# Kernel optimization log

Hardware: AMD Instinct MI355X
Metric: run time of the kernel (lower is better)

Reference implementation:

```python
import jax, jax.numpy as jnp
import numpy as np

B, N, E, H = 8, 2048, 64, 4
D = E * H  # internal width = embedding_dim * num_heads


def _ln(x, g, b):
    m = jnp.mean(x, -1, keepdims=True)
    v = jnp.var(x, -1, keepdims=True)
    return (x - m) / jnp.sqrt(v + 1e-5) * g + b


def setup_inputs() -> dict:
    key = jax.random.key(0)
    ks = jax.random.split(key, 10)

    def lin(k, o, i):
        return jax.random.normal(k, (o, i), jnp.float32) / np.sqrt(i).astype(np.float32)

    return {
        "x": jax.random.normal(ks[0], (B, N, E), jnp.float32),
        "weights": jax.random.uniform(ks[1], (B, N, 1), jnp.float32),
        "ln_g": jnp.ones((E,), jnp.float32),
        "ln_b": jnp.zeros((E,), jnp.float32),
        "wq_w": lin(ks[2], D, E), "wq_b": jnp.zeros((D,), jnp.float32),
        "wk_w": lin(ks[3], D, E), "wk_b": jnp.zeros((D,), jnp.float32),
        "wv_w": lin(ks[4], D, E), "wv_b": jnp.zeros((D,), jnp.float32),
        "mq_w": lin(ks[5], D, D), "mq_b": jnp.zeros((D,), jnp.float32),
        "mk_w": lin(ks[6], D, D), "mk_b": jnp.zeros((D,), jnp.float32),
        "out_w": lin(ks[7], E, D), "out_b": jnp.zeros((E,), jnp.float32),
        "ffn_w": lin(ks[8], E, E), "ffn_b": jnp.zeros((E,), jnp.float32),
    }


def reference(x, weights, ln_g, ln_b, wq_w, wq_b, wk_w, wk_b, wv_w, wv_b,
              mq_w, mq_b, mk_w, mk_b, out_w, out_b, ffn_w, ffn_b):
    Bn, Nn, En = x.shape
    Dd = mq_w.shape[0]
    Hh = Dd // En  # head_dim == embedding_dim in this module

    x_norm = _ln(x, ln_g, ln_b)
    # outer W_q/W_k then nn.MultiheadAttention in-projections (q,k only; v/out_proj are dead)
    q = (x_norm @ wq_w.T + wq_b) @ mq_w.T + mq_b  # [B,N,D]
    k = (x_norm @ wk_w.T + wk_b) @ mk_w.T + mk_b  # [B,N,D]
    q = q.reshape(Bn, Nn, Hh, En)
    k = k.reshape(Bn, Nn, Hh, En)

    scale = np.float32(1.0 / np.sqrt(En))
    scores = jnp.einsum('bihe,bjhe->bhij', q, k) * scale  # [B,H,N,N]
    pad = jnp.sum(weights, -1) == 0.0  # [B,N] key_padding_mask
    scores = jnp.where(pad[:, None, None, :], jnp.float32(-1e9), scores)
    att = jax.nn.softmax(scores, axis=-1).mean(axis=1)  # averaged over heads: [B,N,N]

    # re-weight by input weights and renormalize (second softmax-like pass)
    att = att * weights[..., 0][:, None, :]
    att = att / jnp.sum(att, -1, keepdims=True)

    v = x_norm @ wv_w.T + wv_b  # fresh W_v(x_norm), NOT MHA's value path
    att_out = jnp.einsum('bij,bjd->bid', att, v)  # [B,N,D]

    out1 = x + att_out @ out_w.T + out_b  # [B,N,E]
    out2 = jax.nn.softplus(_ln(out1, ln_g, ln_b) @ ffn_w.T + ffn_b)
    return _ln(out1 + out2, ln_g, ln_b)
```

## Files before the change

kernel.cpp:

```cpp
#include <hip/hip_runtime.h>
#include <hip/hip_bf16.h>

#define BB 8
#define NN 2048
#define EE 64
#define DD 256

typedef __attribute__((ext_vector_type(8))) short short8;
typedef __attribute__((ext_vector_type(4))) float f32x4;
typedef __attribute__((ext_vector_type(4))) unsigned short ushort4v;

#define MFMA16(a, b, c) __builtin_amdgcn_mfma_f32_16x16x32_bf16((a), (b), (c), 0, 0, 0)

#if __has_builtin(__builtin_amdgcn_exp2f)
#define EXP2(x) __builtin_amdgcn_exp2f(x)
#else
#define EXP2(x) exp2f(x)
#endif

__device__ inline void gload16(const void* g, void* l) {
  __builtin_amdgcn_global_load_lds(
      (const __attribute__((address_space(1))) unsigned int*)g,
      (__attribute__((address_space(3))) unsigned int*)l, 16, 0, 0);
}

__device__ inline float bf2f(unsigned short u) {
  union { unsigned int i; float f; } v;
  v.i = ((unsigned int)u) << 16;
  return v.f;
}
__device__ inline unsigned short f2bf(float f) {
  union { float f; unsigned int i; } v;
  v.f = f;
  unsigned int r = v.i + 0x7FFFu + ((v.i >> 16) & 1u);
  return (unsigned short)(r >> 16);
}

__global__ __launch_bounds__(128) void kprep(
    const float* __restrict__ wq_w, const float* __restrict__ wq_b,
    const float* __restrict__ wk_w, const float* __restrict__ wk_b,
    const float* __restrict__ wv_w, const float* __restrict__ mq_w,
    const float* __restrict__ mq_b, const float* __restrict__ mk_w,
    const float* __restrict__ mk_b, const float* __restrict__ out_w,
    const float* __restrict__ ffn_w,
    unsigned short* __restrict__ wqc, float* __restrict__ bqc,
    unsigned short* __restrict__ wkc, float* __restrict__ bkc,
    unsigned short* __restrict__ wvc, unsigned short* __restrict__ outwb,
    unsigned short* __restrict__ ffnwb) {
  const float SC = 0.18033688011112042f;
  int o = blockIdx.x;
  int t = threadIdx.x;
  if (t < 64) {
    float acc = 0.f;
#pragma unroll 4
    for (int d = 0; d < 256; d++) acc += mq_w[o * 256 + d] * wq_w[d * 64 + t];
    wqc[o * 64 + t] = f2bf(acc * SC);
  } else {
    int k = t - 64;
    float acc = 0.f;
#pragma unroll 4
    for (int d = 0; d < 256; d++) acc += mk_w[o * 256 + d] * wk_w[d * 64 + k];
    wkc[o * 64 + k] = f2bf(acc);
  }
  if (t == 0) {
    float acc = 0.f;
    for (int d = 0; d < 256; d++) acc += mq_w[o * 256 + d] * wq_b[d];
    bqc[o] = (acc + mq_b[o]) * SC;
  }
  if (t == 64) {
    float acc = 0.f;
    for (int d = 0; d < 256; d++) acc += mk_w[o * 256 + d] * wk_b[d];
    bkc[o] = acc + mk_b[o];
  }
  int gid = o * 128 + t;
  if (gid < 16384) {
    wvc[gid] = f2bf(wv_w[gid]);
    outwb[gid] = f2bf(out_w[gid]);
  }
  if (gid < 4096) ffnwb[gid] = f2bf(ffn_w[gid]);
}

__global__ __launch_bounds__(128, 2) void kproj(
    const float* __restrict__ x, const float* __restrict__ ln_g,
    const float* __restrict__ ln_b, const unsigned short* __restrict__ wqc,
    const float* __restrict__ bqc, const unsigned short* __restrict__ wkc,
    const float* __restrict__ bkc, const unsigned short* __restrict__ wvc,
    const float* __restrict__ wv_b, unsigned short* __restrict__ qout,
    unsigned short* __restrict__ kout, unsigned short* __restrict__ vtout) {
  __shared__ __align__(1024) char lds[2 * 10240];
  int tid = threadIdx.x;
  int w = tid >> 6, l = tid & 63;
  int c = l & 15, g = l >> 4;
  int blk = blockIdx.x;
  int b = blk >> 6;
  int i0 = (blk & 63) * 32 + w * 16;
  size_t row0 = (size_t)b * NN + i0;
  char* xnb = lds + w * 10240;
  char* tlb = lds + w * 10240 + 2048;

  int rl = l >> 2;
  int cc = (l & 3) * 16;
  float xv[16];
  {
    const float* xr = x + (row0 + rl) * EE + cc;
#pragma unroll
    for (int i = 0; i < 4; i++) {
      float4 v = *(const float4*)(xr + i * 4);
      xv[i * 4 + 0] = v.x; xv[i * 4 + 1] = v.y;
      xv[i * 4 + 2] = v.z; xv[i * 4 + 3] = v.w;
    }
  }
  float s = 0.f, s2 = 0.f;
#pragma unroll
  for (int i = 0; i < 16; i++) { s += xv[i]; s2 += xv[i] * xv[i]; }
  s += __shfl_xor(s, 1); s += __shfl_xor(s, 2);
  s2 += __shfl_xor(s2, 1); s2 += __shfl_xor(s2, 2);
  float mean = s * (1.f / 64.f);
  float var = s2 * (1.f / 64.f) - mean * mean;
  float rstd = rsqrtf(var + 1e-5f);
  {
    int swzr = (rl & 7) << 4;
    unsigned short pk[16];
#pragma unroll
    for (int i = 0; i < 16; i++)
      pk[i] = f2bf((xv[i] - mean) * rstd * ln_g[cc + i] + ln_b[cc + i]);
#pragma unroll
    for (int hh = 0; hh < 2; hh++) {
      short8 d;
#pragma unroll
      for (int i = 0; i < 8; i++) d[i] = (short)pk[hh * 8 + i];
      *(short8*)(xnb + rl * 128 + (((l & 3) * 32 + hh * 16) ^ swzr)) = d;
    }
  }
  __syncthreads();

  int swz = (c & 7) << 4;
  int o2_0 = (g * 16) ^ swz;
  int o2_1 = (64 + g * 16) ^ swz;
  short8 af0 = *(const short8*)(xnb + c * 128 + o2_0);
  short8 af1 = *(const short8*)(xnb + c * 128 + o2_1);

#pragma unroll
  for (int dt = 0; dt < 16; dt++) {
    float bias = bqc[dt * 16 + c];
    f32x4 acc = {bias, bias, bias, bias};
    acc = MFMA16(af0, *(const short8*)(wqc + (dt * 16 + c) * 64 + g * 8), acc);
    acc = MFMA16(af1, *(const short8*)(wqc + (dt * 16 + c) * 64 + 32 + g * 8), acc);
#pragma unroll
    for (int r = 0; r < 4; r++) {
      int row = 4 * g + r;
      *(unsigned short*)(tlb + row * 512 + ((dt * 32 + 2 * c) ^ ((row & 7) << 4))) = f2bf(acc[r]);
    }
  }
  __syncthreads();
#pragma unroll
  for (int c2 = 0; c2 < 8; c2++) {
    int flat = c2 * 1024 + l * 16;
    int rowt = flat >> 9;
    int off = flat & 511;
    short8 d = *(const short8*)(tlb + rowt * 512 + (off ^ ((rowt & 7) << 4)));
    *(short8*)((char*)qout + (row0 + rowt) * 512 + off) = d;
  }
  __syncthreads();

#pragma unroll
  for (int dt = 0; dt < 16; dt++) {
    float bias = bkc[dt * 16 + c];
    f32x4 acc = {bias, bias, bias, bias};
    acc = MFMA16(af0, *(const short8*)(wkc + (dt * 16 + c) * 64 + g * 8), acc);
    acc = MFMA16(af1, *(const short8*)(wkc + (dt * 16 + c) * 64 + 32 + g * 8), acc);
#pragma unroll
    for (int r = 0; r < 4; r++) {
      int row = 4 * g + r;
      *(unsigned short*)(tlb + row * 512 + ((dt * 32 + 2 * c) ^ ((row & 7) << 4))) = f2bf(acc[r]);
    }
  }
  __syncthreads();
#pragma unroll
  for (int c2 = 0; c2 < 8; c2++) {
    int flat = c2 * 1024 + l * 16;
    int rowt = flat >> 9;
    int off = flat & 511;
    short8 d = *(const short8*)(tlb + rowt * 512 + (off ^ ((rowt & 7) << 4)));
    *(short8*)((char*)kout + (row0 + rowt) * 512 + off) = d;
  }

#pragma unroll
  for (int dt = 0; dt < 16; dt++) {
    float bias = wv_b[dt * 16 + c];
    f32x4 acc = {bias, bias, bias, bias};
    acc = MFMA16(af0, *(const short8*)(wvc + (dt * 16 + c) * 64 + g * 8), acc);
    acc = MFMA16(af1, *(const short8*)(wvc + (dt * 16 + c) * 64 + 32 + g * 8), acc);
    ushort4v pk;
#pragma unroll
    for (int r = 0; r < 4; r++) pk[r] = f2bf(acc[r]);
    *(ushort4v*)(vtout + ((size_t)b * 256 + dt * 16 + c) * NN + i0 + 4 * g) = pk;
  }
}

__global__ __launch_bounds__(512, 2) void kpass1(
    const unsigned short* __restrict__ qb, const unsigned short* __restrict__ kb,
    const float* __restrict__ wts, float* __restrict__ lout) {
  __shared__ __align__(1024) char ldsk[2 * 32768];
  int tid = threadIdx.x;
  int w = tid >> 6, l = tid & 63, c = l & 15, g = l >> 4;
  int p = blockIdx.x;
  int q = (p & 7) * 64 + (p >> 3);
  int y = q >> 7, b = (q >> 4) & 7, it = q & 15;
  int i0 = it * 128 + w * 16;
  const size_t brow = (size_t)b * NN;
  short8 qf[8];
  {
    const unsigned short* qr = qb + (brow + i0 + c) * DD;
#pragma unroll
    for (int s = 0; s < 8; s++) qf[s] = *(const short8*)(qr + s * 32 + g * 8);
  }
  float ls[16];
#pragma unroll
  for (int i = 0; i < 16; i++) ls[i] = 0.f;
  int swz = (c & 7) << 4;
  int o2_0 = (g * 16) ^ swz;
  int o2_1 = (64 + g * 16) ^ swz;

  {
    int jb = y * 512;
#pragma unroll
    for (int call = 0; call < 4; call++) {
      int chunk = call * 512 + tid;
      int j = chunk >> 5;
      int q16 = (chunk & 31) << 4;
      const char* src = (const char*)(kb + (brow + jb + j) * DD) + (q16 ^ ((j & 7) << 4));
      gload16(src, ldsk + (chunk & ~63) * 16);
    }
  }
  for (int jt = 0; jt < 8; jt++) {
    int jb = y * 512 + jt * 64;
    const char* kcur = ldsk + (jt & 1) * 32768;
    char* knxt = ldsk + ((jt + 1) & 1) * 32768;
    __syncthreads();
    if (jt < 7) {
      int jb2 = jb + 64;
#pragma unroll
      for (int call = 0; call < 4; call++) {
        int chunk = call * 512 + tid;
        int j = chunk >> 5;
        int q16 = (chunk & 31) << 4;
        const char* src = (const char*)(kb + (brow + jb2 + j) * DD) + (q16 ^ ((j & 7) << 4));
        gload16(src, knxt + (chunk & ~63) * 16);
      }
    }
    float wm[4];
#pragma unroll
    for (int js = 0; js < 4; js++) {
      float wv = wts[brow + jb + js * 16 + c];
      wm[js] = (wv == 0.f) ? 0.f : 1.f;
    }
    const char* kb0 = kcur + c * 512;
#pragma unroll
    for (int h = 0; h < 4; h++) {
#pragma unroll
      for (int js = 0; js < 4; js++) {
        f32x4 s4 = {0.f, 0.f, 0.f, 0.f};
        s4 = MFMA16(qf[2 * h], *(const short8*)(kb0 + js * 8192 + h * 128 + o2_0), s4);
        s4 = MFMA16(qf[2 * h + 1], *(const short8*)(kb0 + js * 8192 + h * 128 + o2_1), s4);
#pragma unroll
        for (int r = 0; r < 4; r++) ls[h * 4 + r] += EXP2(s4[r]) * wm[js];
      }
    }
  }
#pragma unroll
  for (int xm = 1; xm <= 8; xm <<= 1)
#pragma unroll
    for (int i = 0; i < 16; i++) ls[i] += __shfl_xor(ls[i], xm);
  if (c == 0) {
#pragma unroll
    for (int h = 0; h < 4; h++)
#pragma unroll
      for (int r = 0; r < 4; r++)
        lout[(((size_t)y * BB + b) * 4 + h) * NN + i0 + 4 * g + r] = ls[h * 4 + r];
  }
}

__global__ __launch_bounds__(512, 2) void kpass2(
    const unsigned short* __restrict__ qb, const unsigned short* __restrict__ kb,
    const unsigned short* __restrict__ vt, const float* __restrict__ wts,
    const float* __restrict__ lin_, unsigned short* __restrict__ num,
    float* __restrict__ tout) {
  __shared__ __align__(1024) char lds[2 * 16384 + 2 * 16384 + 8 * 1280];
  int tid = threadIdx.x;
  int w = tid >> 6, l = tid & 63, c = l & 15, g = l >> 4;
  char* ldsk = lds;
  char* ldsv = lds + 32768;
  char* ldsp = lds + 65536 + w * 1280;
  int p = blockIdx.x;
  int q = (p & 7) * 64 + (p >> 3);
  int y = q >> 7, b = (q >> 4) & 7, it = q & 15;
  int i0 = it * 128 + w * 16;
  const size_t brow = (size_t)b * NN;

  float nl[16];
#pragma unroll
  for (int h = 0; h < 4; h++)
#pragma unroll
    for (int r = 0; r < 4; r++) {
      float lsum = 0.f;
#pragma unroll
      for (int yy = 0; yy < 4; yy++)
        lsum += lin_[(((size_t)yy * BB + b) * 4 + h) * NN + i0 + 4 * g + r];
      nl[h * 4 + r] = -log2f(lsum);
    }

  short8 qf[8];
  {
    const unsigned short* qr = qb + (brow + i0 + c) * DD;
#pragma unroll
    for (int s = 0; s < 8; s++) qf[s] = *(const short8*)(qr + s * 32 + g * 8);
  }
  f32x4 acc[16];
#pragma unroll
  for (int i = 0; i < 16; i++) acc[i] = (f32x4){0.f, 0.f, 0.f, 0.f};
  float tacc[4] = {0.f, 0.f, 0.f, 0.f};
  int swz = (c & 7) << 4;
  int o2_0 = (g * 16) ^ swz;
  int o2_1 = (64 + g * 16) ^ swz;
  int pw[8];
#pragma unroll
  for (int js = 0; js < 2; js++)
#pragma unroll
    for (int r = 0; r < 4; r++) pw[js * 4 + r] = (4 * g + r) * 80 + js * 32 + 2 * c;
  const char* prd = ldsp + c * 80 + g * 16;

  {
    int jb = y * 512;
#pragma unroll
    for (int call = 0; call < 2; call++) {
      int chunk = call * 512 + tid;
      int j = chunk >> 5;
      int q16 = (chunk & 31) << 4;
      const char* src = (const char*)(kb + (brow + jb + j) * DD) + (q16 ^ ((j & 7) << 4));
      gload16(src, ldsk + (chunk & ~63) * 16);
    }
#pragma unroll
    for (int call = 0; call < 2; call++) {
      int i = call * 512 + tid;
      int cc = i & 15, joct = (i >> 4) & 3, dt2 = i >> 6;
      const char* src = (const char*)(vt + ((size_t)b * 256 + dt2 * 16 + cc) * NN + jb + joct * 8);
      gload16(src, ldsv + (i & ~63) * 16);
    }
  }

  for (int jt = 0; jt < 16; jt++) {
    int jb = y * 512 + jt * 32;
    const char* kcur = ldsk + (jt & 1) * 16384;
    const char* vcur = ldsv + (jt & 1) * 16384;
    char* knxt = ldsk + ((jt + 1) & 1) * 16384;
    char* vnxt = ldsv + ((jt + 1) & 1) * 16384;
    __syncthreads();
    if (jt < 15) {
      int jb2 = jb + 32;
#pragma unroll
      for (int call = 0; call < 2; call++) {
        int chunk = call * 512 + tid;
        int j = chunk >> 5;
        int q16 = (chunk & 31) << 4;
        const char* src = (const char*)(kb + (brow + jb2 + j) * DD) + (q16 ^ ((j & 7) << 4));
        gload16(src, knxt + (chunk & ~63) * 16);
      }
#pragma unroll
      for (int call = 0; call < 2; call++) {
        int i = call * 512 + tid;
        int cc = i & 15, joct = (i >> 4) & 3, dt2 = i >> 6;
        const char* src = (const char*)(vt + ((size_t)b * 256 + dt2 * 16 + cc) * NN + jb2 + joct * 8);
        gload16(src, vnxt + (i & ~63) * 16);
      }
    }
    float wj[2];
#pragma unroll
    for (int js = 0; js < 2; js++) wj[js] = wts[brow + jb + js * 16 + c];
    const char* kb0 = kcur + c * 512;
    const char* vb0 = vcur + c * 16;
    float av[2][4];
#pragma unroll
    for (int js = 0; js < 2; js++) {
#pragma unroll
      for (int r = 0; r < 4; r++) av[js][r] = 0.f;
#pragma unroll
      for (int h = 0; h < 4; h++) {
        f32x4 s4 = {nl[h * 4 + 0], nl[h * 4 + 1], nl[h * 4 + 2], nl[h * 4 + 3]};
        s4 = MFMA16(qf[2 * h], *(const short8*)(kb0 + js * 8192 + h * 128 + o2_0), s4);
        s4 = MFMA16(qf[2 * h + 1], *(const short8*)(kb0 + js * 8192 + h * 128 + o2_1), s4);
#pragma unroll
        for (int r = 0; r < 4; r++) av[js][r] += EXP2(s4[r]);
      }
#pragma unroll
      for (int r = 0; r < 4; r++) { av[js][r] *= wj[js]; tacc[r] += av[js][r]; }
    }
#pragma unroll
    for (int js = 0; js < 2; js++)
#pragma unroll
      for (int r = 0; r < 4; r++)
        *(unsigned short*)(ldsp + pw[js * 4 + r]) = f2bf(av[js][r]);
    asm volatile("s_waitcnt lgkmcnt(0)" ::: "memory");
    __builtin_amdgcn_sched_barrier(0);
    short8 pf = *(const short8*)prd;
#pragma unroll
    for (int dt = 0; dt < 16; dt++) {
      short8 vf = *(const short8*)(vb0 + dt * 1024 + g * 256);
      acc[dt] = MFMA16(pf, vf, acc[dt]);
    }
  }
#pragma unroll
  for (int xm = 1; xm <= 8; xm <<= 1)
#pragma unroll
    for (int r = 0; r < 4; r++) tacc[r] += __shfl_xor(tacc[r], xm);
#pragma unroll
  for (int dt = 0; dt < 16; dt++)
#pragma unroll
    for (int r = 0; r < 4; r++)
      num[(((size_t)y * BB + b) * NN + i0 + 4 * g + r) * DD + dt * 16 + c] = f2bf(acc[dt][r]);
  if (c == 0)
#pragma unroll
    for (int r = 0; r < 4; r++)
      tout[((size_t)y * BB + b) * NN + i0 + 4 * g + r] = tacc[r];
}

__global__ __launch_bounds__(128, 2) void kfinal(
    const unsigned short* __restrict__ num, const float* __restrict__ tws,
    const float* __restrict__ x, const unsigned short* __restrict__ outwb,
    const float* __restrict__ out_b, const float* __restrict__ ln_g,
    const float* __restrict__ ln_b, const unsigned short* __restrict__ ffnwb,
    const float* __restrict__ ffn_b, float* __restrict__ out) {
  __shared__ __align__(1024) char lds[2 * 2304];
  int tid = threadIdx.x, w = tid >> 6, l = tid & 63, c = l & 15, g = l >> 4;
  int blk = blockIdx.x;
  int b = blk >> 6;
  int i0 = (blk & 63) * 32 + w * 16;
  char* hb = lds + w * 2304;

  short8 af[8];
  {
    const unsigned short* p0 = num + (((size_t)0 * BB + b) * NN + i0 + c) * DD;
    const unsigned short* p1 = num + (((size_t)1 * BB + b) * NN + i0 + c) * DD;
    const unsigned short* p2 = num + (((size_t)2 * BB + b) * NN + i0 + c) * DD;
    const unsigned short* p3 = num + (((size_t)3 * BB + b) * NN + i0 + c) * DD;
#pragma unroll
    for (int s = 0; s < 8; s++) {
      short8 a0 = *(const short8*)(p0 + s * 32 + g * 8);
      short8 a1 = *(const short8*)(p1 + s * 32 + g * 8);
      short8 a2 = *(const short8*)(p2 + s * 32 + g * 8);
      short8 a3 = *(const short8*)(p3 + s * 32 + g * 8);
      short8 o;
#pragma unroll
      for (int t2 = 0; t2 < 8; t2++)
        o[t2] = (short)f2bf(bf2f((unsigned short)a0[t2]) + bf2f((unsigned short)a1[t2]) +
                            bf2f((unsigned short)a2[t2]) + bf2f((unsigned short)a3[t2]));
      af[s] = o;
    }
  }
  float trow[4];
#pragma unroll
  for (int r = 0; r < 4; r++) {
    trow[r] = 0.f;
#pragma unroll
    for (int yy = 0; yy < 4; yy++)
      trow[r] += tws[((size_t)yy * BB + b) * NN + i0 + 4 * g + r];
  }
  f32x4 acc[4];
#pragma unroll
  for (int ct = 0; ct < 4; ct++) {
    acc[ct] = (f32x4){0.f, 0.f, 0.f, 0.f};
#pragma unroll
    for (int s = 0; s < 8; s++)
      acc[ct] = MFMA16(af[s], *(const short8*)(outwb + (ct * 16 + c) * DD + s * 32 + g * 8), acc[ct]);
  }
  float gv[4], bvv[4], obv[4], fbv[4];
#pragma unroll
  for (int ct = 0; ct < 4; ct++) {
    gv[ct] = ln_g[ct * 16 + c]; bvv[ct] = ln_b[ct * 16 + c];
    obv[ct] = out_b[ct * 16 + c]; fbv[ct] = ffn_b[ct * 16 + c];
  }
  float o1[4][4];
#pragma unroll
  for (int ct = 0; ct < 4; ct++)
#pragma unroll
    for (int r = 0; r < 4; r++)
      o1[ct][r] = x[((size_t)b * NN + i0 + 4 * g + r) * EE + ct * 16 + c] +
                  acc[ct][r] / trow[r] + obv[ct];
  float h1[4][4];
#pragma unroll
  for (int r = 0; r < 4; r++) {
    float s = o1[0][r] + o1[1][r] + o1[2][r] + o1[3][r];
    float s2 = o1[0][r] * o1[0][r] + o1[1][r] * o1[1][r] +
               o1[2][r] * o1[2][r] + o1[3][r] * o1[3][r];
#pragma unroll
    for (int xm = 1; xm < 16; xm <<= 1) { s += __shfl_xor(s, xm); s2 += __shfl_xor(s2, xm); }
    float mean = s * (1.f / 64.f);
    float var = s2 * (1.f / 64.f) - mean * mean;
    float rstd = rsqrtf(var + 1e-5f);
#pragma unroll
    for (int ct = 0; ct < 4; ct++)
      h1[ct][r] = (o1[ct][r] - mean) * rstd * gv[ct] + bvv[ct];
  }
#pragma unroll
  for (int ct = 0; ct < 4; ct++)
#pragma unroll
    for (int r = 0; r < 4; r++)
      *(unsigned short*)(hb + (4 * g + r) * 144 + ct * 32 + 2 * c) = f2bf(h1[ct][r]);
  asm volatile("s_waitcnt lgkmcnt(0)" ::: "memory");
  __builtin_amdgcn_sched_barrier(0);
  short8 hf0 = *(const short8*)(hb + c * 144 + g * 16);
  short8 hf1 = *(const short8*)(hb + c * 144 + 64 + g * 16);
  f32x4 a2[4];
#pragma unroll
  for (int ct = 0; ct < 4; ct++) {
    a2[ct] = (f32x4){0.f, 0.f, 0.f, 0.f};
    a2[ct] = MFMA16(hf0, *(const short8*)(ffnwb + (ct * 16 + c) * EE + g * 8), a2[ct]);
    a2[ct] = MFMA16(hf1, *(const short8*)(ffnwb + (ct * 16 + c) * EE + 32 + g * 8), a2[ct]);
  }
  float o3[4][4];
#pragma unroll
  for (int ct = 0; ct < 4; ct++)
#pragma unroll
    for (int r = 0; r < 4; r++) {
      float vv = a2[ct][r] + fbv[ct];
      float sp = fmaxf(vv, 0.f) + log1pf(expf(-fabsf(vv)));
      o3[ct][r] = o1[ct][r] + sp;
    }
#pragma unroll
  for (int r = 0; r < 4; r++) {
    float s = o3[0][r] + o3[1][r] + o3[2][r] + o3[3][r];
    float s2 = o3[0][r] * o3[0][r] + o3[1][r] * o3[1][r] +
               o3[2][r] * o3[2][r] + o3[3][r] * o3[3][r];
#pragma unroll
    for (int xm = 1; xm < 16; xm <<= 1) { s += __shfl_xor(s, xm); s2 += __shfl_xor(s2, xm); }
    float mean = s * (1.f / 64.f);
    float var = s2 * (1.f / 64.f) - mean * mean;
    float rstd = rsqrtf(var + 1e-5f);
#pragma unroll
    for (int ct = 0; ct < 4; ct++)
      out[((size_t)b * NN + i0 + 4 * g + r) * EE + ct * 16 + c] =
          (o3[ct][r] - mean) * rstd * gv[ct] + bvv[ct];
  }
}

extern "C" void kernel_launch(void* const* d_in, const int* in_sizes, int n_in,
                              void* d_out, int out_size, void* d_ws, size_t ws_size,
                              hipStream_t stream) {
  (void)in_sizes; (void)n_in; (void)out_size; (void)ws_size;
  const float* x = (const float*)d_in[0];
  const float* wts = (const float*)d_in[1];
  const float* ln_g = (const float*)d_in[2];
  const float* ln_b = (const float*)d_in[3];
  const float* wq_w = (const float*)d_in[4];
  const float* wq_b = (const float*)d_in[5];
  const float* wk_w = (const float*)d_in[6];
  const float* wk_b = (const float*)d_in[7];
  const float* wv_w = (const float*)d_in[8];
  const float* wv_b = (const float*)d_in[9];
  const float* mq_w = (const float*)d_in[10];
  const float* mq_b = (const float*)d_in[11];
  const float* mk_w = (const float*)d_in[12];
  const float* mk_b = (const float*)d_in[13];
  const float* out_w = (const float*)d_in[14];
  const float* out_b = (const float*)d_in[15];
  const float* ffn_w = (const float*)d_in[16];
  const float* ffn_b = (const float*)d_in[17];
  float* out = (float*)d_out;

  char* ws = (char*)d_ws;
  unsigned short* qb = (unsigned short*)(ws + 0);
  unsigned short* kb = (unsigned short*)(ws + 8388608);
  unsigned short* vt = (unsigned short*)(ws + 16777216);
  float* l1 = (float*)(ws + 25165824);
  unsigned short* num = (unsigned short*)(ws + 26214400);
  float* tws = (float*)(ws + 59768832);
  unsigned short* wqc = (unsigned short*)(ws + 60030976);
  unsigned short* wkc = (unsigned short*)(ws + 60063744);
  unsigned short* wvc = (unsigned short*)(ws + 60096512);
  float* bqc = (float*)(ws + 60129280);
  float* bkc = (float*)(ws + 60130304);
  unsigned short* outwb = (unsigned short*)(ws + 60131328);
  unsigned short* ffnwb = (unsigned short*)(ws + 60164096);

  kprep<<<256, 128, 0, stream>>>(wq_w, wq_b, wk_w, wk_b, wv_w, mq_w, mq_b,
                                 mk_w, mk_b, out_w, ffn_w, wqc, bqc, wkc, bkc,
                                 wvc, outwb, ffnwb);
  kproj<<<512, 128, 0, stream>>>(x, ln_g, ln_b, wqc, bqc, wkc, bkc, wvc, wv_b,
                                 qb, kb, vt);
  kpass1<<<512, 512, 0, stream>>>(qb, kb, wts, l1);
  kpass2<<<512, 512, 0, stream>>>(qb, kb, vt, wts, l1, num, tws);
  kfinal<<<512, 128, 0, stream>>>(num, tws, x, outwb, out_b, ln_g, ln_b, ffnwb,
                                  ffn_b, out);
}
```

Measured before the change: 255.4 us.

## Retile attention passes so each wave reuses key fragments across two query tiles

Both attention passes move to 256-thread blocks and twice as many blocks. Each wave now covers 32 query rows and half of the key tile, so every K fragment read from LDS feeds two query tiles. In pass2 the P tile is shared between wave pairs through LDS with a barrier, and each wave accumulates half of the value dimension. The softmax normalisation changes from a log2 bias to a multiply by the inverse row sum, and the partial-sum buffers grow from 4 to 8 slices. The cost is more K/V loading per query row, because each block holds fewer query rows, plus an extra block barrier per tile.

```diff
diff --git a/kernel.cpp b/kernel.cpp
--- a/kernel.cpp
+++ b/kernel.cpp
@@ -198,26 +198,33 @@
   }
 }
 
-__global__ __launch_bounds__(512, 2) void kpass1(
+__global__ __launch_bounds__(256, 2) void kpass1(
     const unsigned short* __restrict__ qb, const unsigned short* __restrict__ kb,
     const float* __restrict__ wts, float* __restrict__ lout) {
   __shared__ __align__(1024) char ldsk[2 * 32768];
   int tid = threadIdx.x;
   int w = tid >> 6, l = tid & 63, c = l & 15, g = l >> 4;
+  int pr = w >> 1, sub = w & 1;
   int p = blockIdx.x;
-  int q = (p & 7) * 64 + (p >> 3);
-  int y = q >> 7, b = (q >> 4) & 7, it = q & 15;
-  int i0 = it * 128 + w * 16;
+  int q = (p & 7) * 128 + (p >> 3);
+  int y = q >> 8, b = (q >> 5) & 7, it = q & 31;
+  int i0 = it * 64 + pr * 32;
   const size_t brow = (size_t)b * NN;
-  short8 qf[8];
-  {
-    const unsigned short* qr = qb + (brow + i0 + c) * DD;
-#pragma unroll
-    for (int s = 0; s < 8; s++) qf[s] = *(const short8*)(qr + s * 32 + g * 8);
-  }
-  float ls[16];
-#pragma unroll
-  for (int i = 0; i < 16; i++) ls[i] = 0.f;
+
+  short8 qf[2][8];
+#pragma unroll
+  for (int t2 = 0; t2 < 2; t2++) {
+    const unsigned short* qr = qb + (brow + i0 + t2 * 16 + c) * DD;
+#pragma unroll
+    for (int s = 0; s < 8; s++) qf[t2][s] = *(const short8*)(qr + s * 32 + g * 8);
+  }
+  float ls[4][2][4];
+#pragma unroll
+  for (int h = 0; h < 4; h++)
+#pragma unroll
+    for (int t2 = 0; t2 < 2; t2++)
+#pragma unroll
+      for (int r = 0; r < 4; r++) ls[h][t2][r] = 0.f;
   int swz = (c & 7) << 4;
   int o2_0 = (g * 16) ^ swz;
   int o2_1 = (64 + g * 16) ^ swz;
@@ -225,8 +232,8 @@
   {
     int jb = y * 512;
 #pragma unroll
-    for (int call = 0; call < 4; call++) {
-      int chunk = call * 512 + tid;
+    for (int call = 0; call < 8; call++) {
+      int chunk = call * 256 + tid;
       int j = chunk >> 5;
       int q16 = (chunk & 31) << 4;
       const char* src = (const char*)(kb + (brow + jb + j) * DD) + (q16 ^ ((j & 7) << 4));
@@ -241,108 +248,120 @@
     if (jt < 7) {
       int jb2 = jb + 64;
 #pragma unroll
-      for (int call = 0; call < 4; call++) {
-        int chunk = call * 512 + tid;
+      for (int call = 0; call < 8; call++) {
+        int chunk = call * 256 + tid;
         int j = chunk >> 5;
         int q16 = (chunk & 31) << 4;
         const char* src = (const char*)(kb + (brow + jb2 + j) * DD) + (q16 ^ ((j & 7) << 4));
         gload16(src, knxt + (chunk & ~63) * 16);
       }
     }
-    float wm[4];
-#pragma unroll
-    for (int js = 0; js < 4; js++) {
-      float wv = wts[brow + jb + js * 16 + c];
-      wm[js] = (wv == 0.f) ? 0.f : 1.f;
-    }
-    const char* kb0 = kcur + c * 512;
+    float wm[2];
+#pragma unroll
+    for (int jt2 = 0; jt2 < 2; jt2++) {
+      float wv = wts[brow + jb + sub * 32 + jt2 * 16 + c];
+      wm[jt2] = (wv == 0.f) ? 0.f : 1.f;
+    }
 #pragma unroll
     for (int h = 0; h < 4; h++) {
 #pragma unroll
-      for (int js = 0; js < 4; js++) {
-        f32x4 s4 = {0.f, 0.f, 0.f, 0.f};
-        s4 = MFMA16(qf[2 * h], *(const short8*)(kb0 + js * 8192 + h * 128 + o2_0), s4);
-        s4 = MFMA16(qf[2 * h + 1], *(const short8*)(kb0 + js * 8192 + h * 128 + o2_1), s4);
-#pragma unroll
-        for (int r = 0; r < 4; r++) ls[h * 4 + r] += EXP2(s4[r]) * wm[js];
+      for (int jt2 = 0; jt2 < 2; jt2++) {
+        const char* kr = kcur + (sub * 32 + jt2 * 16 + c) * 512;
+        short8 b0 = *(const short8*)(kr + h * 128 + o2_0);
+        short8 b1 = *(const short8*)(kr + h * 128 + o2_1);
+#pragma unroll
+        for (int t2 = 0; t2 < 2; t2++) {
+          f32x4 s4 = {0.f, 0.f, 0.f, 0.f};
+          s4 = MFMA16(qf[t2][2 * h], b0, s4);
+          s4 = MFMA16(qf[t2][2 * h + 1], b1, s4);
+#pragma unroll
+          for (int r = 0; r < 4; r++) ls[h][t2][r] += EXP2(s4[r]) * wm[jt2];
+        }
       }
     }
   }
 #pragma unroll
   for (int xm = 1; xm <= 8; xm <<= 1)
 #pragma unroll
-    for (int i = 0; i < 16; i++) ls[i] += __shfl_xor(ls[i], xm);
+    for (int h = 0; h < 4; h++)
+#pragma unroll
+      for (int t2 = 0; t2 < 2; t2++)
+#pragma unroll
+        for (int r = 0; r < 4; r++) ls[h][t2][r] += __shfl_xor(ls[h][t2][r], xm);
   if (c == 0) {
 #pragma unroll
     for (int h = 0; h < 4; h++)
 #pragma unroll
-      for (int r = 0; r < 4; r++)
-        lout[(((size_t)y * BB + b) * 4 + h) * NN + i0 + 4 * g + r] = ls[h * 4 + r];
-  }
-}
-
-__global__ __launch_bounds__(512, 2) void kpass2(
+      for (int t2 = 0; t2 < 2; t2++)
+#pragma unroll
+        for (int r = 0; r < 4; r++)
+          lout[(((size_t)(y * 2 + sub) * BB + b) * 4 + h) * NN + i0 + t2 * 16 + 4 * g + r] =
+              ls[h][t2][r];
+  }
+}
+
+__global__ __launch_bounds__(256, 2) void kpass2(
     const unsigned short* __restrict__ qb, const unsigned short* __restrict__ kb,
     const unsigned short* __restrict__ vt, const float* __restrict__ wts,
     const float* __restrict__ lin_, unsigned short* __restrict__ num,
     float* __restrict__ tout) {
-  __shared__ __align__(1024) char lds[2 * 16384 + 2 * 16384 + 8 * 1280];
+  __shared__ __align__(1024) char lds[2 * 16384 + 2 * 16384 + 5120];
   int tid = threadIdx.x;
   int w = tid >> 6, l = tid & 63, c = l & 15, g = l >> 4;
   char* ldsk = lds;
   char* ldsv = lds + 32768;
-  char* ldsp = lds + 65536 + w * 1280;
+  char* ldsp = lds + 65536;
+  int pr = w >> 1, sub = w & 1;
   int p = blockIdx.x;
-  int q = (p & 7) * 64 + (p >> 3);
-  int y = q >> 7, b = (q >> 4) & 7, it = q & 15;
-  int i0 = it * 128 + w * 16;
+  int q = (p & 7) * 128 + (p >> 3);
+  int y = q >> 8, b = (q >> 5) & 7, it = q & 31;
+  int i0 = it * 64 + pr * 32;
   const size_t brow = (size_t)b * NN;
 
-  float nl[16];
+  float invl[4][2][4];
 #pragma unroll
   for (int h = 0; h < 4; h++)
 #pragma unroll
-    for (int r = 0; r < 4; r++) {
-      float lsum = 0.f;
-#pragma unroll
-      for (int yy = 0; yy < 4; yy++)
-        lsum += lin_[(((size_t)yy * BB + b) * 4 + h) * NN + i0 + 4 * g + r];
-      nl[h * 4 + r] = -log2f(lsum);
-    }
-
-  short8 qf[8];
-  {
-    const unsigned short* qr = qb + (brow + i0 + c) * DD;
-#pragma unroll
-    for (int s = 0; s < 8; s++) qf[s] = *(const short8*)(qr + s * 32 + g * 8);
-  }
-  f32x4 acc[16];
-#pragma unroll
-  for (int i = 0; i < 16; i++) acc[i] = (f32x4){0.f, 0.f, 0.f, 0.f};
-  float tacc[4] = {0.f, 0.f, 0.f, 0.f};
+    for (int t2 = 0; t2 < 2; t2++)
+#pragma unroll
+      for (int r = 0; r < 4; r++) {
+        float lsum = 0.f;
+#pragma unroll
+        for (int yy = 0; yy < 8; yy++)
+          lsum += lin_[(((size_t)yy * BB + b) * 4 + h) * NN + i0 + t2 * 16 + 4 * g + r];
+        invl[h][t2][r] = 1.f / lsum;
+      }
+
+  short8 qf[2][8];
+#pragma unroll
+  for (int t2 = 0; t2 < 2; t2++) {
+    const unsigned short* qr = qb + (brow + i0 + t2 * 16 + c) * DD;
+#pragma unroll
+    for (int s = 0; s < 8; s++) qf[t2][s] = *(const short8*)(qr + s * 32 + g * 8);
+  }
+  f32x4 acc[2][8];
+#pragma unroll
+  for (int t2 = 0; t2 < 2; t2++)
+#pragma unroll
+    for (int dt = 0; dt < 8; dt++) acc[t2][dt] = (f32x4){0.f, 0.f, 0.f, 0.f};
+  float tacc[2][4] = {{0.f, 0.f, 0.f, 0.f}, {0.f, 0.f, 0.f, 0.f}};
   int swz = (c & 7) << 4;
   int o2_0 = (g * 16) ^ swz;
   int o2_1 = (64 + g * 16) ^ swz;
-  int pw[8];
-#pragma unroll
-  for (int js = 0; js < 2; js++)
-#pragma unroll
-    for (int r = 0; r < 4; r++) pw[js * 4 + r] = (4 * g + r) * 80 + js * 32 + 2 * c;
-  const char* prd = ldsp + c * 80 + g * 16;
 
   {
     int jb = y * 512;
 #pragma unroll
-    for (int call = 0; call < 2; call++) {
-      int chunk = call * 512 + tid;
+    for (int call = 0; call < 4; call++) {
+      int chunk = call * 256 + tid;
       int j = chunk >> 5;
       int q16 = (chunk & 31) << 4;
       const char* src = (const char*)(kb + (brow + jb + j) * DD) + (q16 ^ ((j & 7) << 4));
       gload16(src, ldsk + (chunk & ~63) * 16);
     }
 #pragma unroll
-    for (int call = 0; call < 2; call++) {
-      int i = call * 512 + tid;
+    for (int call = 0; call < 4; call++) {
+      int i = call * 256 + tid;
       int cc = i & 15, joct = (i >> 4) & 3, dt2 = i >> 6;
       const char* src = (const char*)(vt + ((size_t)b * 256 + dt2 * 16 + cc) * NN + jb + joct * 8);
       gload16(src, ldsv + (i & ~63) * 16);
@@ -359,69 +378,80 @@
     if (jt < 15) {
       int jb2 = jb + 32;
 #pragma unroll
-      for (int call = 0; call < 2; call++) {
-        int chunk = call * 512 + tid;
+      for (int call = 0; call < 4; call++) {
+        int chunk = call * 256 + tid;
         int j = chunk >> 5;
         int q16 = (chunk & 31) << 4;
         const char* src = (const char*)(kb + (brow + jb2 + j) * DD) + (q16 ^ ((j & 7) << 4));
         gload16(src, knxt + (chunk & ~63) * 16);
       }
 #pragma unroll
-      for (int call = 0; call < 2; call++) {
-        int i = call * 512 + tid;
+      for (int call = 0; call < 4; call++) {
+        int i = call * 256 + tid;
         int cc = i & 15, joct = (i >> 4) & 3, dt2 = i >> 6;
         const char* src = (const char*)(vt + ((size_t)b * 256 + dt2 * 16 + cc) * NN + jb2 + joct * 8);
         gload16(src, vnxt + (i & ~63) * 16);
       }
     }
-    float wj[2];
-#pragma unroll
-    for (int js = 0; js < 2; js++) wj[js] = wts[brow + jb + js * 16 + c];
-    const char* kb0 = kcur + c * 512;
-    const char* vb0 = vcur + c * 16;
-    float av[2][4];
-#pragma unroll
-    for (int js = 0; js < 2; js++) {
-#pragma unroll
-      for (int r = 0; r < 4; r++) av[js][r] = 0.f;
-#pragma unroll
-      for (int h = 0; h < 4; h++) {
-        f32x4 s4 = {nl[h * 4 + 0], nl[h * 4 + 1], nl[h * 4 + 2], nl[h * 4 + 3]};
-        s4 = MFMA16(qf[2 * h], *(const short8*)(kb0 + js * 8192 + h * 128 + o2_0), s4);
-        s4 = MFMA16(qf[2 * h + 1], *(const short8*)(kb0 + js * 8192 + h * 128 + o2_1), s4);
-#pragma unroll
-        for (int r = 0; r < 4; r++) av[js][r] += EXP2(s4[r]);
+    float wj = wts[brow + jb + sub * 16 + c];
+    const char* kr = kcur + (sub * 16 + c) * 512;
+    float av[2][4] = {{0.f, 0.f, 0.f, 0.f}, {0.f, 0.f, 0.f, 0.f}};
+#pragma unroll
+    for (int h = 0; h < 4; h++) {
+      short8 b0 = *(const short8*)(kr + h * 128 + o2_0);
+      short8 b1 = *(const short8*)(kr + h * 128 + o2_1);
+#pragma unroll
+      for (int t2 = 0; t2 < 2; t2++) {
+        f32x4 s4 = {0.f, 0.f, 0.f, 0.f};
+        s4 = MFMA16(qf[t2][2 * h], b0, s4);
+        s4 = MFMA16(qf[t2][2 * h + 1], b1, s4);
+#pragma unroll
+        for (int r = 0; r < 4; r++) av[t2][r] += EXP2(s4[r]) * invl[h][t2][r];
       }
-#pragma unroll
-      for (int r = 0; r < 4; r++) { av[js][r] *= wj[js]; tacc[r] += av[js][r]; }
-    }
-#pragma unroll
-    for (int js = 0; js < 2; js++)
+    }
+#pragma unroll
+    for (int t2 = 0; t2 < 2; t2++)
+#pragma unroll
+      for (int r = 0; r < 4; r++) {
+        av[t2][r] *= wj;
+        tacc[t2][r] += av[t2][r];
+        *(unsigned short*)(ldsp + ((size_t)(pr * 32 + t2 * 16 + 4 * g + r)) * 80 +
+                           (sub * 16 + c) * 2) = f2bf(av[t2][r]);
+      }
+    asm volatile("s_waitcnt lgkmcnt(0)" ::: "memory");
+    __builtin_amdgcn_s_barrier();
+    asm volatile("" ::: "memory");
+    __builtin_amdgcn_sched_barrier(0);
+    short8 pf0 = *(const short8*)(ldsp + (pr * 32 + c) * 80 + g * 16);
+    short8 pf1 = *(const short8*)(ldsp + (pr * 32 + 16 + c) * 80 + g * 16);
+    const char* vb = vcur + sub * 8192 + g * 256 + c * 16;
+#pragma unroll
+    for (int dt = 0; dt < 8; dt++) {
+      short8 vf = *(const short8*)(vb + dt * 1024);
+      acc[0][dt] = MFMA16(pf0, vf, acc[0][dt]);
+      acc[1][dt] = MFMA16(pf1, vf, acc[1][dt]);
+    }
+  }
+#pragma unroll
+  for (int xm = 1; xm <= 8; xm <<= 1)
+#pragma unroll
+    for (int t2 = 0; t2 < 2; t2++)
+#pragma unroll
+      for (int r = 0; r < 4; r++) tacc[t2][r] += __shfl_xor(tacc[t2][r], xm);
+#pragma unroll
+  for (int t2 = 0; t2 < 2; t2++)
+#pragma unroll
+    for (int dt = 0; dt < 8; dt++)
 #pragma unroll
       for (int r = 0; r < 4; r++)
-        *(unsigned short*)(ldsp + pw[js * 4 + r]) = f2bf(av[js][r]);
-    asm volatile("s_waitcnt lgkmcnt(0)" ::: "memory");
-    __builtin_amdgcn_sched_barrier(0);
-    short8 pf = *(const short8*)prd;
-#pragma unroll
-    for (int dt = 0; dt < 16; dt++) {
-      short8 vf = *(const short8*)(vb0 + dt * 1024 + g * 256);
-      acc[dt] = MFMA16(pf, vf, acc[dt]);
-    }
-  }
-#pragma unroll
-  for (int xm = 1; xm <= 8; xm <<= 1)
-#pragma unroll
-    for (int r = 0; r < 4; r++) tacc[r] += __shfl_xor(tacc[r], xm);
-#pragma unroll
-  for (int dt = 0; dt < 16; dt++)
-#pragma unroll
-    for (int r = 0; r < 4; r++)
-      num[(((size_t)y * BB + b) * NN + i0 + 4 * g + r) * DD + dt * 16 + c] = f2bf(acc[dt][r]);
+        num[(((size_t)y * BB + b) * NN + i0 + t2 * 16 + 4 * g + r) * DD + sub * 128 +
+            dt * 16 + c] = f2bf(acc[t2][dt][r]);
   if (c == 0)
 #pragma unroll
-    for (int r = 0; r < 4; r++)
-      tout[((size_t)y * BB + b) * NN + i0 + 4 * g + r] = tacc[r];
+    for (int t2 = 0; t2 < 2; t2++)
+#pragma unroll
+      for (int r = 0; r < 4; r++)
+        tout[((size_t)(y * 2 + sub) * BB + b) * NN + i0 + t2 * 16 + 4 * g + r] = tacc[t2][r];
 }
 
 __global__ __launch_bounds__(128, 2) void kfinal(
@@ -462,7 +492,7 @@
   for (int r = 0; r < 4; r++) {
     trow[r] = 0.f;
 #pragma unroll
-    for (int yy = 0; yy < 4; yy++)
+    for (int yy = 0; yy < 8; yy++)
       trow[r] += tws[((size_t)yy * BB + b) * NN + i0 + 4 * g + r];
   }
   f32x4 acc[4];
@@ -572,23 +602,23 @@
   unsigned short* kb = (unsigned short*)(ws + 8388608);
   unsigned short* vt = (unsigned short*)(ws + 16777216);
   float* l1 = (float*)(ws + 25165824);
-  unsigned short* num = (unsigned short*)(ws + 26214400);
-  float* tws = (float*)(ws + 59768832);
-  unsigned short* wqc = (unsigned short*)(ws + 60030976);
-  unsigned short* wkc = (unsigned short*)(ws + 60063744);
-  unsigned short* wvc = (unsigned short*)(ws + 60096512);
-  float* bqc = (float*)(ws + 60129280);
-  float* bkc = (float*)(ws + 60130304);
-  unsigned short* outwb = (unsigned short*)(ws + 60131328);
-  unsigned short* ffnwb = (unsigned short*)(ws + 60164096);
+  unsigned short* num = (unsigned short*)(ws + 27262976);
+  float* tws = (float*)(ws + 60817408);
+  unsigned short* wqc = (unsigned short*)(ws + 61341696);
+  unsigned short* wkc = (unsigned short*)(ws + 61374464);
+  unsigned short* wvc = (unsigned short*)(ws + 61407232);
+  float* bqc = (float*)(ws + 61440000);
+  float* bkc = (float*)(ws + 61441024);
+  unsigned short* outwb = (unsigned short*)(ws + 61442048);
+  unsigned short* ffnwb = (unsigned short*)(ws + 61474816);
 
   kprep<<<256, 128, 0, stream>>>(wq_w, wq_b, wk_w, wk_b, wv_w, mq_w, mq_b,
                                  mk_w, mk_b, out_w, ffn_w, wqc, bqc, wkc, bkc,
                                  wvc, outwb, ffnwb);
   kproj<<<512, 128, 0, stream>>>(x, ln_g, ln_b, wqc, bqc, wkc, bkc, wvc, wv_b,
                                  qb, kb, vt);
-  kpass1<<<512, 512, 0, stream>>>(qb, kb, wts, l1);
-  kpass2<<<512, 512, 0, stream>>>(qb, kb, vt, wts, l1, num, tws);
+  kpass1<<<1024, 256, 0, stream>>>(qb, kb, wts, l1);
+  kpass2<<<1024, 256, 0, stream>>>(qb, kb, vt, wts, l1, num, tws);
   kfinal<<<512, 128, 0, stream>>>(num, tws, x, outwb, out_b, ln_g, ln_b, ffnwb,
                                   ffn_b, out);
 }
```

Result: no change. 254.0 us (-0.6%).

## Retile pass1 so wave pairs share K fragments; coalesce partial-sum loads in final kernel

Applied to the files above, without the earlier changes.

In the first attention pass, each wave now handles 32 query rows and half of each 64-key tile instead of 16 rows over the full tile. Each K fragment read from LDS therefore feeds two MFMAs, halving LDS traffic per MFMA. The cost is twice as many row-sum partials (8 slices instead of 4), which pass2 now sums and which need a larger l1 workspace, so later buffers shift. The final kernel also loads the four bf16 numerator partials with coalesced flat reads, reduces them, and stages the result in swizzled LDS before building MFMA fragments. This replaces strided per-lane row loads at the price of an extra barrier and LDS round trip.

```diff
diff --git a/kernel.cpp b/kernel.cpp
--- a/kernel.cpp
+++ b/kernel.cpp
@@ -204,20 +204,27 @@
   __shared__ __align__(1024) char ldsk[2 * 32768];
   int tid = threadIdx.x;
   int w = tid >> 6, l = tid & 63, c = l & 15, g = l >> 4;
+  int pr = w >> 1, sub = w & 1;
   int p = blockIdx.x;
   int q = (p & 7) * 64 + (p >> 3);
   int y = q >> 7, b = (q >> 4) & 7, it = q & 15;
-  int i0 = it * 128 + w * 16;
+  int i0 = it * 128 + pr * 32;
   const size_t brow = (size_t)b * NN;
-  short8 qf[8];
-  {
-    const unsigned short* qr = qb + (brow + i0 + c) * DD;
-#pragma unroll
-    for (int s = 0; s < 8; s++) qf[s] = *(const short8*)(qr + s * 32 + g * 8);
-  }
-  float ls[16];
-#pragma unroll
-  for (int i = 0; i < 16; i++) ls[i] = 0.f;
+
+  short8 qf[2][8];
+#pragma unroll
+  for (int t2 = 0; t2 < 2; t2++) {
+    const unsigned short* qr = qb + (brow + i0 + t2 * 16 + c) * DD;
+#pragma unroll
+    for (int s = 0; s < 8; s++) qf[t2][s] = *(const short8*)(qr + s * 32 + g * 8);
+  }
+  float ls[4][2][4];
+#pragma unroll
+  for (int h = 0; h < 4; h++)
+#pragma unroll
+    for (int t2 = 0; t2 < 2; t2++)
+#pragma unroll
+      for (int r = 0; r < 4; r++) ls[h][t2][r] = 0.f;
   int swz = (c & 7) << 4;
   int o2_0 = (g * 16) ^ swz;
   int o2_1 = (64 + g * 16) ^ swz;
@@ -249,35 +256,47 @@
         gload16(src, knxt + (chunk & ~63) * 16);
       }
     }
-    float wm[4];
-#pragma unroll
-    for (int js = 0; js < 4; js++) {
-      float wv = wts[brow + jb + js * 16 + c];
-      wm[js] = (wv == 0.f) ? 0.f : 1.f;
-    }
-    const char* kb0 = kcur + c * 512;
+    float wm[2];
+#pragma unroll
+    for (int jt2 = 0; jt2 < 2; jt2++) {
+      float wv = wts[brow + jb + sub * 32 + jt2 * 16 + c];
+      wm[jt2] = (wv == 0.f) ? 0.f : 1.f;
+    }
 #pragma unroll
     for (int h = 0; h < 4; h++) {
 #pragma unroll
-      for (int js = 0; js < 4; js++) {
-        f32x4 s4 = {0.f, 0.f, 0.f, 0.f};
-        s4 = MFMA16(qf[2 * h], *(const short8*)(kb0 + js * 8192 + h * 128 + o2_0), s4);
-        s4 = MFMA16(qf[2 * h + 1], *(const short8*)(kb0 + js * 8192 + h * 128 + o2_1), s4);
-#pragma unroll
-        for (int r = 0; r < 4; r++) ls[h * 4 + r] += EXP2(s4[r]) * wm[js];
+      for (int jt2 = 0; jt2 < 2; jt2++) {
+        const char* kr = kcur + (sub * 32 + jt2 * 16 + c) * 512;
+        short8 b0 = *(const short8*)(kr + h * 128 + o2_0);
+        short8 b1 = *(const short8*)(kr + h * 128 + o2_1);
+#pragma unroll
+        for (int t2 = 0; t2 < 2; t2++) {
+          f32x4 s4 = {0.f, 0.f, 0.f, 0.f};
+          s4 = MFMA16(qf[t2][2 * h], b0, s4);
+          s4 = MFMA16(qf[t2][2 * h + 1], b1, s4);
+#pragma unroll
+          for (int r = 0; r < 4; r++) ls[h][t2][r] += EXP2(s4[r]) * wm[jt2];
+        }
       }
     }
   }
 #pragma unroll
   for (int xm = 1; xm <= 8; xm <<= 1)
 #pragma unroll
-    for (int i = 0; i < 16; i++) ls[i] += __shfl_xor(ls[i], xm);
+    for (int h = 0; h < 4; h++)
+#pragma unroll
+      for (int t2 = 0; t2 < 2; t2++)
+#pragma unroll
+        for (int r = 0; r < 4; r++) ls[h][t2][r] += __shfl_xor(ls[h][t2][r], xm);
   if (c == 0) {
 #pragma unroll
     for (int h = 0; h < 4; h++)
 #pragma unroll
-      for (int r = 0; r < 4; r++)
-        lout[(((size_t)y * BB + b) * 4 + h) * NN + i0 + 4 * g + r] = ls[h * 4 + r];
+      for (int t2 = 0; t2 < 2; t2++)
+#pragma unroll
+        for (int r = 0; r < 4; r++)
+          lout[(((size_t)(y * 2 + sub) * BB + b) * 4 + h) * NN + i0 + t2 * 16 + 4 * g + r] =
+              ls[h][t2][r];
   }
 }
 
@@ -305,7 +324,7 @@
     for (int r = 0; r < 4; r++) {
       float lsum = 0.f;
 #pragma unroll
-      for (int yy = 0; yy < 4; yy++)
+      for (int yy = 0; yy < 8; yy++)
         lsum += lin_[(((size_t)yy * BB + b) * 4 + h) * NN + i0 + 4 * g + r];
       nl[h * 4 + r] = -log2f(lsum);
     }
@@ -430,32 +449,44 @@
     const float* __restrict__ out_b, const float* __restrict__ ln_g,
     const float* __restrict__ ln_b, const unsigned short* __restrict__ ffnwb,
     const float* __restrict__ ffn_b, float* __restrict__ out) {
-  __shared__ __align__(1024) char lds[2 * 2304];
+  __shared__ __align__(1024) char lds[16384 + 2 * 2304];
   int tid = threadIdx.x, w = tid >> 6, l = tid & 63, c = l & 15, g = l >> 4;
   int blk = blockIdx.x;
   int b = blk >> 6;
-  int i0 = (blk & 63) * 32 + w * 16;
-  char* hb = lds + w * 2304;
-
-  short8 af[8];
+  int i0t = (blk & 63) * 32;
+  int i0 = i0t + w * 16;
+  char* nb = lds;
+  char* hb = lds + 16384 + w * 2304;
+
   {
-    const unsigned short* p0 = num + (((size_t)0 * BB + b) * NN + i0 + c) * DD;
-    const unsigned short* p1 = num + (((size_t)1 * BB + b) * NN + i0 + c) * DD;
-    const unsigned short* p2 = num + (((size_t)2 * BB + b) * NN + i0 + c) * DD;
-    const unsigned short* p3 = num + (((size_t)3 * BB + b) * NN + i0 + c) * DD;
-#pragma unroll
-    for (int s = 0; s < 8; s++) {
-      short8 a0 = *(const short8*)(p0 + s * 32 + g * 8);
-      short8 a1 = *(const short8*)(p1 + s * 32 + g * 8);
-      short8 a2 = *(const short8*)(p2 + s * 32 + g * 8);
-      short8 a3 = *(const short8*)(p3 + s * 32 + g * 8);
+    const size_t slice = (size_t)BB * NN * DD;
+    const unsigned short* nbase = num + ((size_t)b * NN + i0t) * DD;
+#pragma unroll
+    for (int sw = 0; sw < 8; sw++) {
+      int flat = sw * 1024 + tid * 8;
+      short8 a0 = *(const short8*)(nbase + 0 * slice + flat);
+      short8 a1 = *(const short8*)(nbase + 1 * slice + flat);
+      short8 a2 = *(const short8*)(nbase + 2 * slice + flat);
+      short8 a3 = *(const short8*)(nbase + 3 * slice + flat);
       short8 o;
 #pragma unroll
       for (int t2 = 0; t2 < 8; t2++)
         o[t2] = (short)f2bf(bf2f((unsigned short)a0[t2]) + bf2f((unsigned short)a1[t2]) +
                             bf2f((unsigned short)a2[t2]) + bf2f((unsigned short)a3[t2]));
-      af[s] = o;
-    }
+      int row = flat >> 8;
+      int off = (flat & 255) * 2;
+      *(short8*)(nb + row * 512 + (off ^ ((row & 15) << 4))) = o;
+    }
+  }
+  __syncthreads();
+
+  short8 af[8];
+  {
+    int row = w * 16 + c;
+    int swzr = (row & 15) << 4;
+#pragma unroll
+    for (int s = 0; s < 8; s++)
+      af[s] = *(const short8*)(nb + row * 512 + ((s * 64 + g * 16) ^ swzr));
   }
   float trow[4];
 #pragma unroll
@@ -572,15 +603,15 @@
   unsigned short* kb = (unsigned short*)(ws + 8388608);
   unsigned short* vt = (unsigned short*)(ws + 16777216);
   float* l1 = (float*)(ws + 25165824);
-  unsigned short* num = (unsigned short*)(ws + 26214400);
-  float* tws = (float*)(ws + 59768832);
-  unsigned short* wqc = (unsigned short*)(ws + 60030976);
-  unsigned short* wkc = (unsigned short*)(ws + 60063744);
-  unsigned short* wvc = (unsigned short*)(ws + 60096512);
-  float* bqc = (float*)(ws + 60129280);
-  float* bkc = (float*)(ws + 60130304);
-  unsigned short* outwb = (unsigned short*)(ws + 60131328);
-  unsigned short* ffnwb = (unsigned short*)(ws + 60164096);
+  unsigned short* num = (unsigned short*)(ws + 27262976);
+  float* tws = (float*)(ws + 60817408);
+  unsigned short* wqc = (unsigned short*)(ws + 61341696);
+  unsigned short* wkc = (unsigned short*)(ws + 61374464);
+  unsigned short* wvc = (unsigned short*)(ws + 61407232);
+  float* bqc = (float*)(ws + 61440000);
+  float* bkc = (float*)(ws + 61441024);
+  unsigned short* outwb = (unsigned short*)(ws + 61442048);
+  unsigned short* ffnwb = (unsigned short*)(ws + 61474816);
 
   kprep<<<256, 128, 0, stream>>>(wq_w, wq_b, wk_w, wk_b, wv_w, mq_w, mq_b,
                                  mk_w, mk_b, out_w, ffn_w, wqc, bqc, wkc, bkc,
```

Result: no change. 251.6 us (-1.5%).
